# Kernel tuning notes

Hardware: AMD Instinct MI355X
Metric: run time of the kernel (lower is better)

Reference implementation:

```python
import jax, jax.numpy as jnp
import numpy as np

D = 512      # model_dim
H = 8        # num_heads
HD = D // H  # head_dim = 64
S = 196      # tokens per channel (14x14 grid)
CHANNELS = np.array([2, 4, 6, 4], dtype=np.int32)  # multiplex channels per sample


def setup_inputs() -> dict:
    key = jax.random.key(0)
    ks = jax.random.split(key, 8)
    C = int(CHANNELS.sum())  # 16
    n = lambda k, shp, s=1.0: jax.random.normal(k, shp, dtype=jnp.float32) * s
    return {
        "x_query": n(ks[0], (C, S, D)),
        "x_keyval": n(ks[1], (C, S, D)),
        "pos": n(ks[2], (C, S, D)),
        "channels": CHANNELS,
        "Wq": n(ks[3], (D, D), 0.02), "bq": jnp.zeros((D,), jnp.float32),
        "Wk": n(ks[4], (D, D), 0.02), "bk": jnp.zeros((D,), jnp.float32),
        "Wv": n(ks[5], (D, D), 0.02), "bv": jnp.zeros((D,), jnp.float32),
        "Wo": n(ks[6], (D, D), 0.02), "bo": jnp.zeros((D,), jnp.float32),
    }


def reference(x_query, x_keyval, pos, channels, Wq, bq, Wk, bk, Wv, bv, Wo, bo):
    C, S_, D_ = x_query.shape
    ch = np.asarray(channels)
    # segment id per packed token; segment i has length channels[i]*S (== cu_seq_len blocks)
    seg = np.repeat(np.arange(ch.shape[0]), ch * S_)                # [T] static
    block_mask = seg[:, None] == seg[None, :]                        # [T,T] static bool

    xq = x_query.reshape(-1, D_)   # [T,D]
    xk = x_keyval.reshape(-1, D_)
    p = pos.reshape(-1, D_)

    # positional embedding fused into Q/K before projection (query_pos/key_pos)
    q = ((xq + p) @ Wq + bq).reshape(-1, H, HD)
    k = ((xk + p) @ Wk + bk).reshape(-1, H, HD)
    v = (xk @ Wv + bv).reshape(-1, H, HD)

    scale = 1.0 / np.sqrt(HD)
    scores = jnp.einsum('qhd,khd->hqk', q, k) * scale               # [H,T,T]
    scores = jnp.where(block_mask[None], scores, jnp.float32(-1e30))
    attn = jax.nn.softmax(scores, axis=-1)
    out = jnp.einsum('hqk,khd->qhd', attn, v).reshape(-1, D_)       # [T,D]
    out = out @ Wo + bo
    return out.reshape(C, S_, D_)
```

## Files before the change

kernel.cpp:

```cpp
#include <hip/hip_runtime.h>


typedef short short8 __attribute__((ext_vector_type(8)));
typedef float f32x4 __attribute__((ext_vector_type(4)));

__device__ __forceinline__ float b2f(unsigned short u) {
    union { float f; unsigned int i; } x; x.i = ((unsigned int)u) << 16; return x.f;
}
__device__ __forceinline__ unsigned short f2b(float f) {
    union { float f; unsigned int i; } x; x.f = f;
    unsigned int r = x.i + 0x7fffu + ((x.i >> 16) & 1u);
    return (unsigned short)(r >> 16);
}

#define NE 1605632
#define WE 262144
#define GS 72

__launch_bounds__(256)
__global__ void prep(const float* __restrict__ xq, const float* __restrict__ xk,
                     const float* __restrict__ pos,
                     const float* __restrict__ W0, const float* __restrict__ W1,
                     const float* __restrict__ W2, const float* __restrict__ W3,
                     unsigned short* __restrict__ WF,
                     unsigned short* __restrict__ aqb, unsigned short* __restrict__ akb,
                     unsigned short* __restrict__ xkbb) {
    const int tid = threadIdx.x;
    if (blockIdx.z < 4) {
        if (blockIdx.x >= 128) return;
        const float* W = blockIdx.z == 0 ? W0 : blockIdx.z == 1 ? W1 : blockIdx.z == 2 ? W2 : W3;
        unsigned short* T = WF + (size_t)blockIdx.z * WE;
        const int s = blockIdx.x * 4 + (tid >> 6);
        const int f = s >> 4, t = s & 15;
        const int lane = tid & 63, quad = lane >> 4, l16 = lane & 15;
        short8 o;
        #pragma unroll
        for (int j = 0; j < 8; ++j)
            o[j] = (short)f2b(W[(size_t)(t * 32 + quad * 8 + j) * 512 + f * 16 + l16]);
        *(short8*)(T + (size_t)s * 512 + lane * 8) = o;
    } else {
        const size_t e = ((size_t)blockIdx.x * 256 + tid) * 8;
        f32x4 q0 = *(const f32x4*)(xq + e),  q1 = *(const f32x4*)(xq + e + 4);
        f32x4 k0 = *(const f32x4*)(xk + e),  k1 = *(const f32x4*)(xk + e + 4);
        f32x4 p0 = *(const f32x4*)(pos + e), p1 = *(const f32x4*)(pos + e + 4);
        short8 a, b, c;
        #pragma unroll
        for (int j = 0; j < 4; ++j) {
            a[j] = (short)f2b(q0[j] + p0[j]); a[4 + j] = (short)f2b(q1[j] + p1[j]);
            b[j] = (short)f2b(k0[j] + p0[j]); b[4 + j] = (short)f2b(k1[j] + p1[j]);
            c[j] = (short)f2b(k0[j]);         c[4 + j] = (short)f2b(k1[j]);
        }
        *(short8*)(aqb + e)  = a;
        *(short8*)(akb + e)  = b;
        *(short8*)(xkbb + e) = c;
    }
}

template <bool OUT_F32>
__device__ __forceinline__ void gemm_wave(const unsigned short* __restrict__ A,
                                          const unsigned short* __restrict__ WFw,
                                          const float* __restrict__ bias,
                                          void* __restrict__ C,
                                          int m0, int n0) {
    const int lane = threadIdx.x & 63;
    const int quad = lane >> 4, l16 = lane & 15;
    const int f0 = n0 >> 4;
    const unsigned short* Arow = A + (size_t)(m0 + l16) * 512 + quad * 8;
    const unsigned short* Bbase = WFw + (size_t)lane * 8;

    f32x4 acc[4] = {};
    #pragma unroll 4
    for (int t = 0; t < 16; ++t) {
        short8 af = *(const short8*)(Arow + t * 32);
        #pragma unroll
        for (int nt = 0; nt < 4; ++nt) {
            short8 bf = *(const short8*)(Bbase + (size_t)((f0 + nt) * 16 + t) * 512);
            acc[nt] = __builtin_amdgcn_mfma_f32_16x16x32_bf16(af, bf, acc[nt], 0, 0, 0);
        }
    }
    #pragma unroll
    for (int nt = 0; nt < 4; ++nt) {
        const int col = n0 + nt * 16 + l16;
        const float bv = bias[col];
        #pragma unroll
        for (int r = 0; r < 4; ++r) {
            const int row = m0 + quad * 4 + r;
            float cv = acc[nt][r] + bv;
            if constexpr (OUT_F32) ((float*)C)[(size_t)row * 512 + col] = cv;
            else ((unsigned short*)C)[(size_t)row * 512 + col] = f2b(cv);
        }
    }
}

__launch_bounds__(256)
__global__ void qkv_gemm(const unsigned short* __restrict__ aqb,
                         const unsigned short* __restrict__ akb,
                         const unsigned short* __restrict__ xkbb,
                         const unsigned short* __restrict__ WF,
                         const float* __restrict__ bq, const float* __restrict__ bk,
                         const float* __restrict__ bv,
                         unsigned short* __restrict__ qb, unsigned short* __restrict__ kb,
                         unsigned short* __restrict__ vb) {
    const unsigned short* A; const unsigned short* WFw; const float* bias; unsigned short* C;
    switch (blockIdx.z) {
        case 0:  A = aqb;  WFw = WF;          bias = bq; C = qb; break;
        case 1:  A = akb;  WFw = WF + WE;     bias = bk; C = kb; break;
        default: A = xkbb; WFw = WF + 2 * WE; bias = bv; C = vb; break;
    }
    gemm_wave<false>(A, WFw, bias, C, blockIdx.x * 64 + (threadIdx.x >> 6) * 16,
                     blockIdx.y * 64);
}

__launch_bounds__(256)
__global__ void out_gemm(const unsigned short* __restrict__ A,
                         const unsigned short* __restrict__ WFo,
                         const float* __restrict__ bo, float* __restrict__ out) {
    gemm_wave<true>(A, WFo, bo, out, blockIdx.x * 64 + (threadIdx.x >> 6) * 16,
                    blockIdx.y * 64);
}

__launch_bounds__(256)
__global__ void attn_seg(const unsigned short* __restrict__ q,
                         const unsigned short* __restrict__ k,
                         const unsigned short* __restrict__ v,
                         unsigned short* __restrict__ o) {
    __shared__ __align__(16) unsigned short Ks[64 * GS];
    __shared__ __align__(16) unsigned short Vt[64 * GS];
    __shared__ __align__(16) unsigned short Pb[4][16 * GS];
    const int bx = blockIdx.x, h = blockIdx.y;
    int off, L, qt;
    if (bx < 7)       { off = 0;    L = 392;  qt = bx; }
    else if (bx < 20) { off = 392;  L = 784;  qt = bx - 7; }
    else if (bx < 39) { off = 1176; L = 1176; qt = bx - 20; }
    else              { off = 2352; L = 784;  qt = bx - 39; }
    const int tid = threadIdx.x;
    const int wave = tid >> 6, lane = tid & 63;
    const int quad = lane >> 4, l16 = lane & 15;
    const int hb = h * 64;
    const int lastr = off + L - 1;

    int qrow = off + qt * 64 + wave * 16 + l16;
    if (qrow > lastr) qrow = lastr;
    short8 aq0 = *(const short8*)(q + (size_t)qrow * 512 + hb + quad * 8);
    short8 aq1 = *(const short8*)(q + (size_t)qrow * 512 + hb + 32 + quad * 8);

    const int skey = tid & 63, sd = (tid >> 6) * 16;
    const int ntiles = (L + 63) >> 6;

    float lrow[4] = {0.f, 0.f, 0.f, 0.f};
    f32x4 oacc[4] = {};

    short8 kr0, kr1, vr0, vr1;
    {
        int krow = off + skey;
        kr0 = *(const short8*)(k + (size_t)krow * 512 + hb + sd);
        kr1 = *(const short8*)(k + (size_t)krow * 512 + hb + sd + 8);
        vr0 = *(const short8*)(v + (size_t)krow * 512 + hb + sd);
        vr1 = *(const short8*)(v + (size_t)krow * 512 + hb + sd + 8);
    }
    for (int b = 0; b < ntiles; ++b) {
        __syncthreads();
        *(short8*)(Ks + skey * GS + sd)     = kr0;
        *(short8*)(Ks + skey * GS + sd + 8) = kr1;
        #pragma unroll
        for (int j = 0; j < 8; ++j) {
            Vt[(sd + j) * GS + skey]     = (unsigned short)vr0[j];
            Vt[(sd + 8 + j) * GS + skey] = (unsigned short)vr1[j];
        }
        __syncthreads();
        if (b + 1 < ntiles) {
            int kk = (b + 1) * 64 + skey;
            int krow = off + (kk < L ? kk : L - 1);
            kr0 = *(const short8*)(k + (size_t)krow * 512 + hb + sd);
            kr1 = *(const short8*)(k + (size_t)krow * 512 + hb + sd + 8);
            vr0 = *(const short8*)(v + (size_t)krow * 512 + hb + sd);
            vr1 = *(const short8*)(v + (size_t)krow * 512 + hb + sd + 8);
        }
        f32x4 s[4];
        #pragma unroll
        for (int g = 0; g < 4; ++g) {
            short8 kb0 = *(const short8*)(Ks + (g * 16 + l16) * GS + quad * 8);
            short8 kb1 = *(const short8*)(Ks + (g * 16 + l16) * GS + 32 + quad * 8);
            f32x4 z = {0.f, 0.f, 0.f, 0.f};
            z = __builtin_amdgcn_mfma_f32_16x16x32_bf16(aq0, kb0, z, 0, 0, 0);
            s[g] = __builtin_amdgcn_mfma_f32_16x16x32_bf16(aq1, kb1, z, 0, 0, 0);
        }
        float p[4][4];
        #pragma unroll
        for (int g = 0; g < 4; ++g) {
            const bool valid = (b * 64 + g * 16 + l16) < L;
            #pragma unroll
            for (int r = 0; r < 4; ++r) {
                p[g][r] = valid ? __expf(fminf(s[g][r] * 0.125f, 30.f)) : 0.f;
                lrow[r] += p[g][r];
            }
        }
        #pragma unroll
        for (int g = 0; g < 4; ++g)
            #pragma unroll
            for (int r = 0; r < 4; ++r)
                Pb[wave][(quad * 4 + r) * GS + g * 16 + l16] = f2b(p[g][r]);
        short8 pa0 = *(const short8*)(Pb[wave] + l16 * GS + quad * 8);
        short8 pa1 = *(const short8*)(Pb[wave] + l16 * GS + 32 + quad * 8);
        #pragma unroll
        for (int nt = 0; nt < 4; ++nt) {
            short8 vf0 = *(const short8*)(Vt + (nt * 16 + l16) * GS + quad * 8);
            short8 vf1 = *(const short8*)(Vt + (nt * 16 + l16) * GS + 32 + quad * 8);
            oacc[nt] = __builtin_amdgcn_mfma_f32_16x16x32_bf16(pa0, vf0, oacc[nt], 0, 0, 0);
            oacc[nt] = __builtin_amdgcn_mfma_f32_16x16x32_bf16(pa1, vf1, oacc[nt], 0, 0, 0);
        }
    }
    #pragma unroll
    for (int r = 0; r < 4; ++r) {
        #pragma unroll
        for (int msk = 1; msk < 16; msk <<= 1)
            lrow[r] += __shfl_xor(lrow[r], msk);
    }
    float linv[4];
    #pragma unroll
    for (int r = 0; r < 4; ++r) linv[r] = 1.0f / lrow[r];
    #pragma unroll
    for (int nt = 0; nt < 4; ++nt) {
        #pragma unroll
        for (int r = 0; r < 4; ++r) {
            const int qi = qt * 64 + wave * 16 + quad * 4 + r;
            if (qi < L)
                o[(size_t)(off + qi) * 512 + hb + nt * 16 + l16] = f2b(oacc[nt][r] * linv[r]);
        }
    }
}

extern "C" void kernel_launch(void* const* d_in, const int* in_sizes, int n_in,
                              void* d_out, int out_size, void* d_ws, size_t ws_size,
                              hipStream_t stream) {
    const float* xq  = (const float*)d_in[0];
    const float* xk  = (const float*)d_in[1];
    const float* pos = (const float*)d_in[2];
    const float* Wq = (const float*)d_in[4];
    const float* bq = (const float*)d_in[5];
    const float* Wk = (const float*)d_in[6];
    const float* bk = (const float*)d_in[7];
    const float* Wv = (const float*)d_in[8];
    const float* bv = (const float*)d_in[9];
    const float* Wo = (const float*)d_in[10];
    const float* bo = (const float*)d_in[11];
    float* out = (float*)d_out;

    unsigned short* ws = (unsigned short*)d_ws;
    unsigned short* qb   = ws;
    unsigned short* kb   = ws + NE;
    unsigned short* vb   = ws + (size_t)2 * NE;
    unsigned short* aqb  = ws + (size_t)3 * NE;
    unsigned short* akb  = ws + (size_t)4 * NE;
    unsigned short* xkbb = ws + (size_t)5 * NE;
    unsigned short* WF   = ws + (size_t)6 * NE;

    prep<<<dim3(784, 1, 5), 256, 0, stream>>>(xq, xk, pos, Wq, Wk, Wv, Wo,
                                              WF, aqb, akb, xkbb);
    qkv_gemm<<<dim3(49, 8, 3), 256, 0, stream>>>(aqb, akb, xkbb, WF, bq, bk, bv,
                                                 qb, kb, vb);
    attn_seg<<<dim3(52, 8), 256, 0, stream>>>(qb, kb, vb, qb);
    out_gemm<<<dim3(49, 8), 256, 0, stream>>>(qb, WF + (size_t)3 * WE, bo, out);
}
```

Baseline: 152.2 us.

## Keep K in registers, compute transposed scores, and schedule long segments first

```diff
diff --git a/kernel.cpp b/kernel.cpp
--- a/kernel.cpp
+++ b/kernel.cpp
@@ -1,4 +1,5 @@
 #include <hip/hip_runtime.h>
+#include <hip/hip_bf16.h>
 
 
 typedef short short8 __attribute__((ext_vector_type(8)));
@@ -124,15 +125,17 @@
                          const unsigned short* __restrict__ k,
                          const unsigned short* __restrict__ v,
                          unsigned short* __restrict__ o) {
-    __shared__ __align__(16) unsigned short Ks[64 * GS];
     __shared__ __align__(16) unsigned short Vt[64 * GS];
-    __shared__ __align__(16) unsigned short Pb[4][16 * GS];
-    const int bx = blockIdx.x, h = blockIdx.y;
-    int off, L, qt;
-    if (bx < 7)       { off = 0;    L = 392;  qt = bx; }
-    else if (bx < 20) { off = 392;  L = 784;  qt = bx - 7; }
-    else if (bx < 39) { off = 1176; L = 1176; qt = bx - 20; }
-    else              { off = 2352; L = 784;  qt = bx - 39; }
+    __shared__ __align__(16) unsigned char  Pw[4][16 * 144];
+
+    const int id = blockIdx.x;
+    int h, off, L, qt;
+    if (id < 152)      { h = id & 7; qt = id >> 3; off = 1176; L = 1176; }
+    else if (id < 360) { int m = id - 152; h = m & 7; int s = m >> 3;
+                         if (s < 13) { off = 392;  L = 784; qt = s; }
+                         else        { off = 2352; L = 784; qt = s - 13; } }
+    else               { int m = id - 360; h = m & 7; qt = m >> 3; off = 0; L = 392; }
+
     const int tid = threadIdx.x;
     const int wave = tid >> 6, lane = tid & 63;
     const int quad = lane >> 4, l16 = lane & 15;
@@ -141,27 +144,36 @@
 
     int qrow = off + qt * 64 + wave * 16 + l16;
     if (qrow > lastr) qrow = lastr;
-    short8 aq0 = *(const short8*)(q + (size_t)qrow * 512 + hb + quad * 8);
-    short8 aq1 = *(const short8*)(q + (size_t)qrow * 512 + hb + 32 + quad * 8);
-
-    const int skey = tid & 63, sd = (tid >> 6) * 16;
+    const short8 qf0 = *(const short8*)(q + (size_t)qrow * 512 + hb + quad * 8);
+    const short8 qf1 = *(const short8*)(q + (size_t)qrow * 512 + hb + 32 + quad * 8);
+
+    const int skey = lane, sd = wave * 16;
     const int ntiles = (L + 63) >> 6;
 
-    float lrow[4] = {0.f, 0.f, 0.f, 0.f};
+    float lsum = 0.f;
     f32x4 oacc[4] = {};
 
-    short8 kr0, kr1, vr0, vr1;
+    const unsigned short* kp = k + (size_t)off * 512 + hb + quad * 8;
+
+    short8 kf[8];
+    short8 vr0, vr1;
     {
+        #pragma unroll
+        for (int g = 0; g < 4; ++g) {
+            const unsigned short* kr = kp + (size_t)(g * 16 + l16) * 512;
+            kf[g * 2]     = *(const short8*)(kr);
+            kf[g * 2 + 1] = *(const short8*)(kr + 32);
+        }
         int krow = off + skey;
-        kr0 = *(const short8*)(k + (size_t)krow * 512 + hb + sd);
-        kr1 = *(const short8*)(k + (size_t)krow * 512 + hb + sd + 8);
         vr0 = *(const short8*)(v + (size_t)krow * 512 + hb + sd);
         vr1 = *(const short8*)(v + (size_t)krow * 512 + hb + sd + 8);
     }
+    unsigned char* Pme = Pw[wave];
+    unsigned char* pwr = Pme + l16 * 144 + quad * 8;
+    const unsigned char* prd = Pme + l16 * 144 + quad * 16;
+
     for (int b = 0; b < ntiles; ++b) {
         __syncthreads();
-        *(short8*)(Ks + skey * GS + sd)     = kr0;
-        *(short8*)(Ks + skey * GS + sd + 8) = kr1;
         #pragma unroll
         for (int j = 0; j < 8; ++j) {
             Vt[(sd + j) * GS + skey]     = (unsigned short)vr0[j];
@@ -171,37 +183,44 @@
         if (b + 1 < ntiles) {
             int kk = (b + 1) * 64 + skey;
             int krow = off + (kk < L ? kk : L - 1);
-            kr0 = *(const short8*)(k + (size_t)krow * 512 + hb + sd);
-            kr1 = *(const short8*)(k + (size_t)krow * 512 + hb + sd + 8);
             vr0 = *(const short8*)(v + (size_t)krow * 512 + hb + sd);
             vr1 = *(const short8*)(v + (size_t)krow * 512 + hb + sd + 8);
         }
-        f32x4 s[4];
+        f32x4 sT[4];
         #pragma unroll
         for (int g = 0; g < 4; ++g) {
-            short8 kb0 = *(const short8*)(Ks + (g * 16 + l16) * GS + quad * 8);
-            short8 kb1 = *(const short8*)(Ks + (g * 16 + l16) * GS + 32 + quad * 8);
             f32x4 z = {0.f, 0.f, 0.f, 0.f};
-            z = __builtin_amdgcn_mfma_f32_16x16x32_bf16(aq0, kb0, z, 0, 0, 0);
-            s[g] = __builtin_amdgcn_mfma_f32_16x16x32_bf16(aq1, kb1, z, 0, 0, 0);
-        }
-        float p[4][4];
+            z     = __builtin_amdgcn_mfma_f32_16x16x32_bf16(kf[g * 2],     qf0, z, 0, 0, 0);
+            sT[g] = __builtin_amdgcn_mfma_f32_16x16x32_bf16(kf[g * 2 + 1], qf1, z, 0, 0, 0);
+        }
+        if (b + 1 < ntiles) {
+            const int nb = (b + 1) * 64;
+            #pragma unroll
+            for (int g = 0; g < 4; ++g) {
+                int kk = nb + g * 16 + l16;
+                const unsigned short* kr = kp + (size_t)(kk < L ? kk : L - 1) * 512;
+                kf[g * 2]     = *(const short8*)(kr);
+                kf[g * 2 + 1] = *(const short8*)(kr + 32);
+            }
+        }
+        const int kbase = b * 64 + quad * 4;
         #pragma unroll
         for (int g = 0; g < 4; ++g) {
-            const bool valid = (b * 64 + g * 16 + l16) < L;
+            float p[4];
             #pragma unroll
             for (int r = 0; r < 4; ++r) {
-                p[g][r] = valid ? __expf(fminf(s[g][r] * 0.125f, 30.f)) : 0.f;
-                lrow[r] += p[g][r];
+                const bool valid = (kbase + g * 16 + r) < L;
+                p[r] = valid ? __expf(fminf(sT[g][r] * 0.125f, 30.f)) : 0.f;
+                lsum += p[r];
             }
-        }
-        #pragma unroll
-        for (int g = 0; g < 4; ++g)
-            #pragma unroll
-            for (int r = 0; r < 4; ++r)
-                Pb[wave][(quad * 4 + r) * GS + g * 16 + l16] = f2b(p[g][r]);
-        short8 pa0 = *(const short8*)(Pb[wave] + l16 * GS + quad * 8);
-        short8 pa1 = *(const short8*)(Pb[wave] + l16 * GS + 32 + quad * 8);
+            #pragma unroll
+            for (int i = 0; i < 2; ++i) {
+                __hip_bfloat162 t = __float22bfloat162_rn(make_float2(p[2 * i], p[2 * i + 1]));
+                *(unsigned int*)(pwr + g * 32 + i * 4) = *(unsigned int*)&t;
+            }
+        }
+        short8 pa0 = *(const short8*)(prd);
+        short8 pa1 = *(const short8*)(prd + 64);
         #pragma unroll
         for (int nt = 0; nt < 4; ++nt) {
             short8 vf0 = *(const short8*)(Vt + (nt * 16 + l16) * GS + quad * 8);
@@ -210,22 +229,17 @@
             oacc[nt] = __builtin_amdgcn_mfma_f32_16x16x32_bf16(pa1, vf1, oacc[nt], 0, 0, 0);
         }
     }
+    lsum += __shfl_xor(lsum, 16);
+    lsum += __shfl_xor(lsum, 32);
     #pragma unroll
     for (int r = 0; r < 4; ++r) {
-        #pragma unroll
-        for (int msk = 1; msk < 16; msk <<= 1)
-            lrow[r] += __shfl_xor(lrow[r], msk);
-    }
-    float linv[4];
-    #pragma unroll
-    for (int r = 0; r < 4; ++r) linv[r] = 1.0f / lrow[r];
-    #pragma unroll
-    for (int nt = 0; nt < 4; ++nt) {
-        #pragma unroll
-        for (int r = 0; r < 4; ++r) {
-            const int qi = qt * 64 + wave * 16 + quad * 4 + r;
-            if (qi < L)
-                o[(size_t)(off + qi) * 512 + hb + nt * 16 + l16] = f2b(oacc[nt][r] * linv[r]);
+        const float srow = __shfl(lsum, (lane & 48) + quad * 4 + r);
+        const float linv = 1.0f / srow;
+        const int qi = qt * 64 + wave * 16 + quad * 4 + r;
+        if (qi < L) {
+            #pragma unroll
+            for (int nt = 0; nt < 4; ++nt)
+                o[(size_t)(off + qi) * 512 + hb + nt * 16 + l16] = f2b(oacc[nt][r] * linv);
         }
     }
 }
@@ -259,6 +273,6 @@
                                               WF, aqb, akb, xkbb);
     qkv_gemm<<<dim3(49, 8, 3), 256, 0, stream>>>(aqb, akb, xkbb, WF, bq, bk, bv,
                                                  qb, kb, vb);
-    attn_seg<<<dim3(52, 8), 256, 0, stream>>>(qb, kb, vb, qb);
+    attn_seg<<<dim3(416), 256, 0, stream>>>(qb, kb, vb, qb);
     out_gemm<<<dim3(49, 8), 256, 0, stream>>>(qb, WF + (size_t)3 * WE, bo, out);
 }
```

Result: slower. 159.8 us (+5.0%).
